# Optimization experiments

Hardware: AMD Instinct MI355X
Metric: run time of the kernel (lower is better)

## Reference

```python
import jax, jax.numpy as jnp
import numpy as np
import math

B, L, D, H, DFF, GEOM = 4, 768, 512, 8, 2048, 7
DK = D // H


def layer_norm(x, scale, bias, eps=1e-5):
    mu = jnp.mean(x, axis=-1, keepdims=True)
    var = jnp.mean(jnp.square(x - mu), axis=-1, keepdims=True)
    return (x - mu) * jax.lax.rsqrt(var + eps) * scale + bias


def setup_inputs() -> dict:
    key = jax.random.key(0)
    ks = jax.random.split(key, 20)
    s = 0.02
    inp = {
        "x": jax.random.normal(ks[0], (B, L, D), jnp.float32),
        "geom_feat": jax.random.uniform(ks[1], (B, L, L, GEOM), jnp.float32),
        "mask": jnp.ones((B, L), jnp.int32),
        # weights stored (in, out): y = x @ W + b, math-equivalent to torch Linear
        "Wq": jax.random.normal(ks[2], (D, D), jnp.float32) * s,
        "bq": jnp.zeros((D,), jnp.float32),
        "Wk": jax.random.normal(ks[3], (D, D), jnp.float32) * s,
        "bk": jnp.zeros((D,), jnp.float32),
        "Wv": jax.random.normal(ks[4], (D, D), jnp.float32) * s,
        "bv": jnp.zeros((D,), jnp.float32),
        "Wo": jax.random.normal(ks[5], (D, D), jnp.float32) * s,
        "bo": jnp.zeros((D,), jnp.float32),
        "Wg": jax.random.normal(ks[6], (GEOM, H), jnp.float32) * s,
        "bg": jnp.zeros((H,), jnp.float32),
        "Wgcn": jax.random.normal(ks[7], (D, D), jnp.float32) * s,
        "bgcn": jnp.zeros((D,), jnp.float32),
        "gcn_gate": jnp.float32(0.5),
        "W1": jax.random.normal(ks[8], (D, 2 * DFF), jnp.float32) * s,
        "b1": jnp.zeros((2 * DFF,), jnp.float32),
        "W2": jax.random.normal(ks[9], (DFF, D), jnp.float32) * s,
        "b2": jnp.zeros((D,), jnp.float32),
        "ln1_s": jnp.ones((D,), jnp.float32),
        "ln1_b": jnp.zeros((D,), jnp.float32),
        "ln2_s": jnp.ones((D,), jnp.float32),
        "ln2_b": jnp.zeros((D,), jnp.float32),
    }
    return inp


def reference(x, geom_feat, mask,
              Wq, bq, Wk, bk, Wv, bv, Wo, bo, Wg, bg,
              Wgcn, bgcn, gcn_gate, W1, b1, W2, b2,
              ln1_s, ln1_b, ln2_s, ln2_b):
    m = mask.astype(x.dtype)  # (B, L)
    # normalized adjacency from distance channel
    adj = jnp.exp(-geom_feat[..., 0] / 5.0)                 # (B, L, L)
    adj = adj * (m[:, :, None] * m[:, None, :])
    adj = adj / (jnp.sum(adj, axis=-1, keepdims=True) + 1e-6)

    h = layer_norm(x, ln1_s, ln1_b)                          # (B, L, D)

    # structure-guided attention
    Q = (h @ Wq + bq).reshape(B, L, H, DK)
    K = (h @ Wk + bk).reshape(B, L, H, DK)
    V = (h @ Wv + bv).reshape(B, L, H, DK)
    scores = jnp.einsum('blhd,bmhd->bhlm', Q, K) / math.sqrt(DK)
    bias = jnp.einsum('blmg,gh->bhlm', geom_feat, Wg) + bg[None, :, None, None]
    scores = scores + bias
    scores = jnp.where(mask[:, None, None, :] == 0, -10000.0, scores)
    attn = jax.nn.softmax(scores, axis=-1)
    ctx = jnp.einsum('bhlm,bmhd->blhd', attn, V).reshape(B, L, D)
    attn_out = ctx @ Wo + bo

    # dense GCN branch (exact GELU, matching torch nn.GELU default)
    g = h @ Wgcn + bgcn
    gcn_out = jax.nn.gelu(jnp.einsum('blm,bmd->bld', adj, g), approximate=False)

    x = x + attn_out + gcn_out * gcn_gate

    # gated feed-forward
    h2 = layer_norm(x, ln2_s, ln2_b)
    ff = h2 @ W1 + b1
    u, gate = ff[..., :DFF], ff[..., DFF:]
    x = x + (u * jax.nn.sigmoid(gate)) @ W2 + b2
    return x
```

## Files before the change

kernel.cpp:

```cpp
#include <hip/hip_runtime.h>
#include <hip/hip_bf16.h>
#include <math.h>

typedef __attribute__((ext_vector_type(8))) short bf8;
typedef __attribute__((ext_vector_type(4))) float f4;

__device__ __forceinline__ ushort f2bf(float x){
  union { float f; unsigned u; } v; v.f = x;
  unsigned r = (v.u + 0x7fffu + ((v.u >> 16) & 1u)) >> 16;
  return (ushort)r;
}
__device__ __forceinline__ float bf2f(ushort b){
  union { unsigned u; float f; } v; v.u = ((unsigned)b) << 16;
  return v.f;
}

struct GP {
  const ushort* A; long lda; long aBatch; long aHead;
  const ushort* Bt; long ldb; long bBatch; long bHead;
  const ushort* Bt2;
  int K; int zdiv;
  float* outf; ushort* outb;
  ushort* o1; ushort* o2; ushort* o3;
  const float* bias0; const float* bias1; const float* bias2; const float* bias3;
  const float* addf;
};

enum { EP_QKVG=0, EP_GCN, EP_ATTNOUT, EP_FF, EP_FINAL };

template<int EPI, bool DUAL>
__global__ __launch_bounds__(256)
void gemm_k(GP p) {
  __shared__ __align__(16) ushort As[64*64];
  __shared__ __align__(16) ushort Bs[64*64];
  __shared__ __align__(16) ushort Bs2[DUAL ? 64*64 : 8];
  const int tid = threadIdx.x;
  const int lane = tid & 63, wave = tid >> 6;
  const int wm = wave >> 1, wn = wave & 1;
  const int bm = blockIdx.x, bn = blockIdx.y, z = blockIdx.z;
  const int zb = z / p.zdiv, zh = z % p.zdiv;
  const ushort* Ab  = p.A  + (long)zb*p.aBatch + (long)zh*p.aHead + (long)bm*64*p.lda;
  const ushort* Btb = p.Bt + (long)zb*p.bBatch + (long)zh*p.bHead + (long)bn*64*p.ldb;
  const ushort* Bt2b = DUAL ? (p.Bt2 + (long)bn*64*p.ldb) : (const ushort*)nullptr;

  f4 acc[2][2] = {};
  f4 acc2[2][2] = {};

  const int sr = tid >> 3, sc = tid & 7;
  const int g = lane >> 4, lr = lane & 15;

  for (int k0 = 0; k0 < p.K; k0 += 64) {
    #pragma unroll
    for (int i = 0; i < 2; ++i) {
      int row = sr + i*32;
      int sw = (sc ^ (row & 7)) * 8;
      *(uint4*)&As[row*64 + sw] = *(const uint4*)(Ab  + (long)row*p.lda + k0 + sc*8);
      *(uint4*)&Bs[row*64 + sw] = *(const uint4*)(Btb + (long)row*p.ldb + k0 + sc*8);
      if (DUAL)
        *(uint4*)&Bs2[row*64 + sw] = *(const uint4*)(Bt2b + (long)row*p.ldb + k0 + sc*8);
    }
    __syncthreads();
    #pragma unroll
    for (int kw = 0; kw < 2; ++kw) {
      bf8 af[2], bfr[2], bf2[2];
      int chunk = kw*4 + g;
      #pragma unroll
      for (int f = 0; f < 2; ++f) {
        int ar = wm*32 + f*16 + lr;
        af[f]  = *(const bf8*)&As[ar*64 + ((chunk ^ (ar & 7)) * 8)];
        int br = wn*32 + f*16 + lr;
        bfr[f] = *(const bf8*)&Bs[br*64 + ((chunk ^ (br & 7)) * 8)];
        if (DUAL) bf2[f] = *(const bf8*)&Bs2[br*64 + ((chunk ^ (br & 7)) * 8)];
      }
      #pragma unroll
      for (int fm = 0; fm < 2; ++fm)
        #pragma unroll
        for (int fn = 0; fn < 2; ++fn) {
          acc[fm][fn] = __builtin_amdgcn_mfma_f32_16x16x32_bf16(af[fm], bfr[fn], acc[fm][fn], 0,0,0);
          if (DUAL) acc2[fm][fn] = __builtin_amdgcn_mfma_f32_16x16x32_bf16(af[fm], bf2[fn], acc2[fm][fn], 0,0,0);
        }
    }
    __syncthreads();
  }

  #pragma unroll
  for (int fm = 0; fm < 2; ++fm)
  #pragma unroll
  for (int fn = 0; fn < 2; ++fn)
  #pragma unroll
  for (int i = 0; i < 4; ++i) {
    int grow = bm*64 + wm*32 + fm*16 + g*4 + i;
    int gcol = bn*64 + wn*32 + fn*16 + lr;
    float v = acc[fm][fn][i];
    if constexpr (EPI == EP_QKVG) {
      int sec = gcol >> 9, cc = gcol & 511;
      const float* bp = sec==0 ? p.bias0 : sec==1 ? p.bias1 : sec==2 ? p.bias2 : p.bias3;
      v += bp[cc];
      ushort bvv = f2bf(v);
      if (sec == 0)      p.outb[(long)grow*512 + cc] = bvv;
      else if (sec == 1) p.o1[(long)grow*512 + cc] = bvv;
      else {
        int b = grow / 768, l = grow - b*768;
        ushort* dst = (sec==2) ? p.o2 : p.o3;
        dst[((long)b*512 + cc)*768 + l] = bvv;
      }
    } else if constexpr (EPI == EP_GCN) {
      float ge = 0.5f * v * (1.f + erff(v * 0.70710678118f));
      p.outf[((long)z*768 + grow)*512 + gcol] = ge;
    } else if constexpr (EPI == EP_ATTNOUT) {
      p.outf[(long)grow*512 + gcol] = v + p.bias0[gcol];
    } else if constexpr (EPI == EP_FF) {
      float u = v + p.bias0[gcol];
      float gt = acc2[fm][fn][i] + p.bias0[2048 + gcol];
      float a = u / (1.f + expf(-gt));
      p.outb[(long)grow*2048 + gcol] = f2bf(a);
    } else if constexpr (EPI == EP_FINAL) {
      long idx = (long)grow*512 + gcol;
      p.outf[idx] = p.addf[idx] + v + p.bias0[gcol];
    }
  }
}

__global__ __launch_bounds__(256) void flash_k(const ushort* __restrict__ qg,
    const ushort* __restrict__ kg, const ushort* __restrict__ vtg,
    const ushort* __restrict__ biasg, ushort* __restrict__ ctx) {
  __shared__ __align__(16) ushort Ks[64*64];
  __shared__ __align__(16) ushort Vs[64*64];
  __shared__ __align__(16) ushort Ps[64*64];
  const int tid = threadIdx.x;
  const int lane = tid & 63, w = tid >> 6;
  const int g = lane >> 4, lr = lane & 15;
  const int qt = blockIdx.x, bh = blockIdx.y;
  const int b = bh >> 3, h = bh & 7;
  const int q0 = qt*64;

  bf8 aq[2];
  #pragma unroll
  for (int kk = 0; kk < 2; ++kk)
    aq[kk] = *(const bf8*)&qg[(long)(b*768 + q0 + w*16 + lr)*512 + h*64 + kk*32 + g*8];

  f4 o[4] = {};
  float mrow[4], lsum[4];
  #pragma unroll
  for (int i = 0; i < 4; ++i) { mrow[i] = -1e30f; lsum[i] = 0.f; }

  const int srow = tid >> 3, sc = tid & 7;

  for (int kt = 0; kt < 12; ++kt) {
    const int kbase = kt*64;
    #pragma unroll
    for (int ps = 0; ps < 2; ++ps) {
      int r = srow + ps*32;
      int sw = ((sc ^ (r & 7)) * 8);
      *(uint4*)&Ks[r*64 + sw] = *(const uint4*)&kg[(long)(b*768 + kbase + r)*512 + h*64 + sc*8];
      *(uint4*)&Vs[r*64 + sw] = *(const uint4*)&vtg[((long)b*512 + h*64 + r)*768 + kbase + sc*8];
    }
    __syncthreads();

    f4 s[4] = {};
    #pragma unroll
    for (int kn = 0; kn < 4; ++kn) {
      #pragma unroll
      for (int kk = 0; kk < 2; ++kk) {
        int row = kn*16 + lr;
        bf8 bk = *(const bf8*)&Ks[row*64 + (((kk*4+g) ^ (row & 7)) * 8)];
        s[kn] = __builtin_amdgcn_mfma_f32_16x16x32_bf16(aq[kk], bk, s[kn], 0,0,0);
      }
    }

    float pv[4][4];
    #pragma unroll
    for (int kn = 0; kn < 4; ++kn)
      #pragma unroll
      for (int i = 0; i < 4; ++i) {
        float bv = bf2f(biasg[((long)bh*768 + q0 + w*16 + g*4 + i)*768 + kbase + kn*16 + lr]);
        pv[kn][i] = s[kn][i]*0.125f + bv;
      }

    #pragma unroll
    for (int i = 0; i < 4; ++i) {
      float m2 = fmaxf(fmaxf(pv[0][i], pv[1][i]), fmaxf(pv[2][i], pv[3][i]));
      #pragma unroll
      for (int off = 1; off < 16; off <<= 1) m2 = fmaxf(m2, __shfl_xor(m2, off, 64));
      float mnew = fmaxf(mrow[i], m2);
      float scale = __expf(mrow[i] - mnew);
      mrow[i] = mnew;
      float psum = 0.f;
      #pragma unroll
      for (int kn = 0; kn < 4; ++kn) { pv[kn][i] = __expf(pv[kn][i] - mnew); psum += pv[kn][i]; }
      #pragma unroll
      for (int off = 1; off < 16; off <<= 1) psum += __shfl_xor(psum, off, 64);
      lsum[i] = lsum[i]*scale + psum;
      #pragma unroll
      for (int dn = 0; dn < 4; ++dn) o[dn][i] *= scale;
    }

    #pragma unroll
    for (int kn = 0; kn < 4; ++kn)
      #pragma unroll
      for (int i = 0; i < 4; ++i) {
        int row = w*16 + g*4 + i;
        int col = kn*16 + lr;
        Ps[row*64 + (((col >> 3) ^ (row & 7)) * 8) + (col & 7)] = f2bf(pv[kn][i]);
      }

    #pragma unroll
    for (int kk2 = 0; kk2 < 2; ++kk2) {
      int prow = w*16 + lr;
      bf8 pa = *(const bf8*)&Ps[prow*64 + (((kk2*4+g) ^ (prow & 7)) * 8)];
      #pragma unroll
      for (int dn = 0; dn < 4; ++dn) {
        int vrow = dn*16 + lr;
        bf8 bv = *(const bf8*)&Vs[vrow*64 + (((kk2*4+g) ^ (vrow & 7)) * 8)];
        o[dn] = __builtin_amdgcn_mfma_f32_16x16x32_bf16(pa, bv, o[dn], 0,0,0);
      }
    }
    __syncthreads();
  }

  #pragma unroll
  for (int i = 0; i < 4; ++i) {
    float inv = 1.f / lsum[i];
    #pragma unroll
    for (int dn = 0; dn < 4; ++dn)
      ctx[(long)(b*768 + q0 + w*16 + g*4 + i)*512 + h*64 + dn*16 + lr] = f2bf(o[dn][i]*inv);
  }
}

__global__ __launch_bounds__(256) void transpose_bf(const float* src, ushort* dst, int R, int C) {
  __shared__ float t[32][33];
  int r0 = blockIdx.x*32, c0 = blockIdx.y*32;
  int tr = threadIdx.x >> 5, tc = threadIdx.x & 31;
  #pragma unroll
  for (int i = 0; i < 4; ++i)
    t[tr + i*8][tc] = src[(long)(r0 + tr + i*8)*C + c0 + tc];
  __syncthreads();
  #pragma unroll
  for (int i = 0; i < 4; ++i)
    dst[(long)(c0 + tr + i*8)*R + r0 + tc] = f2bf(t[tc][tr + i*8]);
}

__global__ __launch_bounds__(256) void ln_k(const float* x, const float* gam, const float* bet, ushort* out) {
  int row = blockIdx.x, tid = threadIdx.x;
  long base = (long)row*512;
  float v0 = x[base+tid], v1 = x[base+tid+256];
  float s = v0+v1, q = v0*v0 + v1*v1;
  #pragma unroll
  for (int off=32; off>=1; off>>=1){ s += __shfl_down(s,off,64); q += __shfl_down(q,off,64); }
  __shared__ float red[8];
  int lane=tid&63, wave=tid>>6;
  if (lane==0){ red[wave]=s; red[4+wave]=q; }
  __syncthreads();
  if (tid==0){ red[0]=red[0]+red[1]+red[2]+red[3]; red[4]=red[4]+red[5]+red[6]+red[7]; }
  __syncthreads();
  float mu = red[0]*(1.f/512.f);
  float var = red[4]*(1.f/512.f) - mu*mu;
  float rs = rsqrtf(var + 1e-5f);
  out[base+tid]     = f2bf((v0-mu)*rs*gam[tid]     + bet[tid]);
  out[base+tid+256] = f2bf((v1-mu)*rs*gam[tid+256] + bet[tid+256]);
}

__global__ __launch_bounds__(256) void resid_ln2_k(const float* x, const float* ao, const float* gc,
    const float* gatep, const float* gam, const float* bet, float* xmid, ushort* h2) {
  int row = blockIdx.x, tid = threadIdx.x;
  long base = (long)row*512;
  float gate = *gatep;
  float v0 = x[base+tid]     + ao[base+tid]     + gc[base+tid]*gate;
  float v1 = x[base+tid+256] + ao[base+tid+256] + gc[base+tid+256]*gate;
  xmid[base+tid] = v0; xmid[base+tid+256] = v1;
  float s = v0+v1, q = v0*v0 + v1*v1;
  #pragma unroll
  for (int off=32; off>=1; off>>=1){ s += __shfl_down(s,off,64); q += __shfl_down(q,off,64); }
  __shared__ float red[8];
  int lane=tid&63, wave=tid>>6;
  if (lane==0){ red[wave]=s; red[4+wave]=q; }
  __syncthreads();
  if (tid==0){ red[0]=red[0]+red[1]+red[2]+red[3]; red[4]=red[4]+red[5]+red[6]+red[7]; }
  __syncthreads();
  float mu = red[0]*(1.f/512.f);
  float var = red[4]*(1.f/512.f) - mu*mu;
  float rs = rsqrtf(var + 1e-5f);
  h2[base+tid]     = f2bf((v0-mu)*rs*gam[tid]     + bet[tid]);
  h2[base+tid+256] = f2bf((v1-mu)*rs*gam[tid+256] + bet[tid+256]);
}

__global__ __launch_bounds__(256) void adjbias_k(const float* __restrict__ geom,
    const int* __restrict__ mask, const float* __restrict__ Wg, const float* __restrict__ bg,
    ushort* __restrict__ adjb, ushort* __restrict__ biasb) {
  int bl = blockIdx.x;
  int b = bl / 768, l = bl - b*768;
  int tid = threadIdx.x;
  __shared__ float wgs[56];
  __shared__ float bgs[8];
  if (tid < 56) wgs[tid] = Wg[tid];
  if (tid < 8)  bgs[tid] = bg[tid];
  __syncthreads();
  float ml = (float)mask[bl];
  float e[3]; float ssum = 0.f;
  #pragma unroll
  for (int j = 0; j < 3; ++j) {
    int m = tid + j*256;
    const float* gp = &geom[((long)bl*768 + m)*7];
    float g0 = gp[0], g1 = gp[1], g2 = gp[2], g3 = gp[3], g4 = gp[4], g5 = gp[5], g6 = gp[6];
    float mm = (float)mask[b*768 + m];
    e[j] = __expf(-g0*0.2f) * mm;
    ssum += e[j];
    #pragma unroll
    for (int hh = 0; hh < 8; ++hh) {
      float bv = bgs[hh] + g0*wgs[hh] + g1*wgs[8+hh] + g2*wgs[16+hh] + g3*wgs[24+hh]
               + g4*wgs[32+hh] + g5*wgs[40+hh] + g6*wgs[48+hh];
      biasb[((long)(b*8+hh)*768 + l)*768 + m] = f2bf(mm != 0.f ? bv : -10000.f);
    }
  }
  #pragma unroll
  for (int off=32; off>=1; off>>=1) ssum += __shfl_down(ssum, off, 64);
  __shared__ float red[4];
  int lane = tid & 63, wave = tid >> 6;
  if (lane == 0) red[wave] = ssum;
  __syncthreads();
  if (tid == 0) red[0] = red[0]+red[1]+red[2]+red[3];
  __syncthreads();
  float inv = ml / (ml*red[0] + 1e-6f);
  #pragma unroll
  for (int j = 0; j < 3; ++j)
    adjb[(long)bl*768 + tid + j*256] = f2bf(e[j] * inv);
}

extern "C" void kernel_launch(void* const* d_in, const int* in_sizes, int n_in,
                              void* d_out, int out_size, void* d_ws, size_t ws_size,
                              hipStream_t stream) {
  const float* x    = (const float*)d_in[0];
  const float* geom = (const float*)d_in[1];
  const int*   mask = (const int*)d_in[2];
  const float* Wq   = (const float*)d_in[3];
  const float* bq   = (const float*)d_in[4];
  const float* Wk   = (const float*)d_in[5];
  const float* bk   = (const float*)d_in[6];
  const float* Wv   = (const float*)d_in[7];
  const float* bv   = (const float*)d_in[8];
  const float* Wo   = (const float*)d_in[9];
  const float* bo   = (const float*)d_in[10];
  const float* Wg   = (const float*)d_in[11];
  const float* bg   = (const float*)d_in[12];
  const float* Wgcn = (const float*)d_in[13];
  const float* bgcn = (const float*)d_in[14];
  const float* gate = (const float*)d_in[15];
  const float* W1   = (const float*)d_in[16];
  const float* b1   = (const float*)d_in[17];
  const float* W2   = (const float*)d_in[18];
  const float* b2   = (const float*)d_in[19];
  const float* ln1s = (const float*)d_in[20];
  const float* ln1b = (const float*)d_in[21];
  const float* ln2s = (const float*)d_in[22];
  const float* ln2b = (const float*)d_in[23];
  float* out = (float*)d_out;

  char* wp = (char*)d_ws;
  auto alloc = [&](size_t bytes)->char* { char* r = wp; wp += (bytes + 255) & ~(size_t)255; return r; };
  ushort* wqkvgT = (ushort*)alloc(2048*512*2);
  ushort* woT    = (ushort*)alloc(512*512*2);
  ushort* w1T    = (ushort*)alloc(4096*512*2);
  ushort* w2T    = (ushort*)alloc(512*2048*2);
  ushort* hbf    = (ushort*)alloc(3072*512*2);
  ushort* qbf    = (ushort*)alloc(3072*512*2);
  ushort* kbf    = (ushort*)alloc(3072*512*2);
  ushort* vt     = (ushort*)alloc((size_t)4*512*768*2);
  ushort* gt     = (ushort*)alloc((size_t)4*512*768*2);
  ushort* adjb   = (ushort*)alloc((size_t)4*768*768*2);
  ushort* biasb  = (ushort*)alloc((size_t)32*768*768*2);
  ushort* ctx    = (ushort*)alloc(3072*512*2);
  float*  aout   = (float*)alloc(3072*512*4);
  float*  gcnr   = (float*)alloc(3072*512*4);
  float*  xmid   = (float*)alloc(3072*512*4);
  ushort* h2bf   = (ushort*)alloc(3072*512*2);
  ushort* act    = biasb;

  transpose_bf<<<dim3(16,16), 256, 0, stream>>>(Wq,   wqkvgT + 0*512*512, 512, 512);
  transpose_bf<<<dim3(16,16), 256, 0, stream>>>(Wk,   wqkvgT + 1*512*512, 512, 512);
  transpose_bf<<<dim3(16,16), 256, 0, stream>>>(Wv,   wqkvgT + 2*512*512, 512, 512);
  transpose_bf<<<dim3(16,16), 256, 0, stream>>>(Wgcn, wqkvgT + 3*512*512, 512, 512);
  transpose_bf<<<dim3(16,16), 256, 0, stream>>>(Wo,   woT, 512, 512);
  transpose_bf<<<dim3(16,128),256, 0, stream>>>(W1,   w1T, 512, 4096);
  transpose_bf<<<dim3(64,16), 256, 0, stream>>>(W2,   w2T, 2048, 512);

  ln_k<<<3072, 256, 0, stream>>>(x, ln1s, ln1b, hbf);

  adjbias_k<<<3072, 256, 0, stream>>>(geom, mask, Wg, bg, adjb, biasb);

  GP p{};
  p.A = hbf; p.lda = 512; p.aBatch = 0; p.aHead = 0;
  p.Bt = wqkvgT; p.ldb = 512; p.bBatch = 0; p.bHead = 0;
  p.K = 512; p.zdiv = 1;
  p.outb = qbf; p.o1 = kbf; p.o2 = vt; p.o3 = gt;
  p.bias0 = bq; p.bias1 = bk; p.bias2 = bv; p.bias3 = bgcn;
  gemm_k<EP_QKVG,false><<<dim3(48,32,1), 256, 0, stream>>>(p);

  flash_k<<<dim3(12,32), 256, 0, stream>>>(qbf, kbf, vt, biasb, ctx);

  p = GP{};
  p.A = adjb; p.lda = 768; p.aBatch = (long)768*768; p.aHead = 0;
  p.Bt = gt; p.ldb = 768; p.bBatch = (long)512*768; p.bHead = 0;
  p.K = 768; p.zdiv = 1;
  p.outf = gcnr;
  gemm_k<EP_GCN,false><<<dim3(12,8,4), 256, 0, stream>>>(p);

  p = GP{};
  p.A = ctx; p.lda = 512; p.aBatch = 0; p.aHead = 0;
  p.Bt = woT; p.ldb = 512; p.bBatch = 0; p.bHead = 0;
  p.K = 512; p.zdiv = 1;
  p.outf = aout; p.bias0 = bo;
  gemm_k<EP_ATTNOUT,false><<<dim3(48,8,1), 256, 0, stream>>>(p);

  resid_ln2_k<<<3072, 256, 0, stream>>>(x, aout, gcnr, gate, ln2s, ln2b, xmid, h2bf);

  p = GP{};
  p.A = h2bf; p.lda = 512; p.aBatch = 0; p.aHead = 0;
  p.Bt = w1T; p.ldb = 512; p.bBatch = 0; p.bHead = 0;
  p.Bt2 = w1T + (long)2048*512;
  p.K = 512; p.zdiv = 1;
  p.outb = act; p.bias0 = b1;
  gemm_k<EP_FF,true><<<dim3(48,32,1), 256, 0, stream>>>(p);

  p = GP{};
  p.A = act; p.lda = 2048; p.aBatch = 0; p.aHead = 0;
  p.Bt = w2T; p.ldb = 2048; p.bBatch = 0; p.bHead = 0;
  p.K = 2048; p.zdiv = 1;
  p.outf = out; p.bias0 = b2; p.addf = xmid;
  gemm_k<EP_FINAL,false><<<dim3(48,8,1), 256, 0, stream>>>(p);
}
```

Before: 313.7 us.

## Enlarge GEMM tiles to 128-row blocks and load tiles via direct global-to-LDS

```diff
diff --git a/kernel.cpp b/kernel.cpp
--- a/kernel.cpp
+++ b/kernel.cpp
@@ -4,6 +4,9 @@
 
 typedef __attribute__((ext_vector_type(8))) short bf8;
 typedef __attribute__((ext_vector_type(4))) float f4;
+
+typedef const __attribute__((address_space(1))) void* gas_t;
+typedef __attribute__((address_space(3))) void* las_t;
 
 __device__ __forceinline__ ushort f2bf(float x){
   union { float f; unsigned u; } v; v.f = x;
@@ -16,10 +19,10 @@
 }
 
 struct GP {
-  const ushort* A; long lda; long aBatch; long aHead;
-  const ushort* Bt; long ldb; long bBatch; long bHead;
+  const ushort* A; long lda; long aBatch;
+  const ushort* Bt; long ldb; long bBatch;
   const ushort* Bt2;
-  int K; int zdiv;
+  int K;
   float* outf; ushort* outb;
   ushort* o1; ushort* o2; ushort* o3;
   const float* bias0; const float* bias1; const float* bias2; const float* bias3;
@@ -28,54 +31,74 @@
 
 enum { EP_QKVG=0, EP_GCN, EP_ATTNOUT, EP_FF, EP_FINAL };
 
-template<int EPI, bool DUAL>
+template<int EPI, bool DUAL, int BN>
 __global__ __launch_bounds__(256)
 void gemm_k(GP p) {
-  __shared__ __align__(16) ushort As[64*64];
-  __shared__ __align__(16) ushort Bs[64*64];
-  __shared__ __align__(16) ushort Bs2[DUAL ? 64*64 : 8];
+  constexpr int WMW = (BN==128) ? 2 : 4;
+  constexpr int WNW = (BN==128) ? 2 : 1;
+  constexpr int WM = 128/WMW, WN = BN/WNW;
+  constexpr int MF = WM/16, NF = WN/16;
+  constexpr int BI = BN/32;
+  __shared__ __align__(16) ushort As[128*64];
+  __shared__ __align__(16) ushort Bs[BN*64];
+  __shared__ __align__(16) ushort Bs2[DUAL ? BN*64 : 8];
   const int tid = threadIdx.x;
-  const int lane = tid & 63, wave = tid >> 6;
-  const int wm = wave >> 1, wn = wave & 1;
+  const int lane = tid & 63, w = tid >> 6;
+  const int wm = (WNW==1) ? w : (w >> 1);
+  const int wn = (WNW==1) ? 0 : (w & 1);
+  const int g = lane >> 4, lr = lane & 15;
+  const int lr8 = lane >> 3, sc = lane & 7;
   const int bm = blockIdx.x, bn = blockIdx.y, z = blockIdx.z;
-  const int zb = z / p.zdiv, zh = z % p.zdiv;
-  const ushort* Ab  = p.A  + (long)zb*p.aBatch + (long)zh*p.aHead + (long)bm*64*p.lda;
-  const ushort* Btb = p.Bt + (long)zb*p.bBatch + (long)zh*p.bHead + (long)bn*64*p.ldb;
-  const ushort* Bt2b = DUAL ? (p.Bt2 + (long)bn*64*p.ldb) : (const ushort*)nullptr;
-
-  f4 acc[2][2] = {};
-  f4 acc2[2][2] = {};
-
-  const int sr = tid >> 3, sc = tid & 7;
-  const int g = lane >> 4, lr = lane & 15;
+
+  const ushort* Ab  = p.A  + (long)z*p.aBatch + (long)bm*128*p.lda;
+  const ushort* Btb = p.Bt + (long)z*p.bBatch + (long)bn*BN*p.ldb;
+  const ushort* Bt2b = DUAL ? (p.Bt2 + (long)bn*BN*p.ldb) : (const ushort*)nullptr;
+
+  f4 acc[MF][NF] = {};
+  f4 acc2[DUAL?MF:1][DUAL?NF:1] = {};
 
   for (int k0 = 0; k0 < p.K; k0 += 64) {
     #pragma unroll
-    for (int i = 0; i < 2; ++i) {
-      int row = sr + i*32;
-      int sw = (sc ^ (row & 7)) * 8;
-      *(uint4*)&As[row*64 + sw] = *(const uint4*)(Ab  + (long)row*p.lda + k0 + sc*8);
-      *(uint4*)&Bs[row*64 + sw] = *(const uint4*)(Btb + (long)row*p.ldb + k0 + sc*8);
-      if (DUAL)
-        *(uint4*)&Bs2[row*64 + sw] = *(const uint4*)(Bt2b + (long)row*p.ldb + k0 + sc*8);
+    for (int i = 0; i < 4; ++i) {
+      int row = i*32 + w*8 + lr8;
+      const ushort* gs = Ab + (long)row*p.lda + k0 + ((sc ^ (row & 7)) << 3);
+      __builtin_amdgcn_global_load_lds((gas_t)gs, (las_t)&As[i*2048 + w*512], 16, 0, 0);
+    }
+    #pragma unroll
+    for (int i = 0; i < BI; ++i) {
+      int row = i*32 + w*8 + lr8;
+      const ushort* gs = Btb + (long)row*p.ldb + k0 + ((sc ^ (row & 7)) << 3);
+      __builtin_amdgcn_global_load_lds((gas_t)gs, (las_t)&Bs[i*2048 + w*512], 16, 0, 0);
+    }
+    if (DUAL) {
+      #pragma unroll
+      for (int i = 0; i < BI; ++i) {
+        int row = i*32 + w*8 + lr8;
+        const ushort* gs = Bt2b + (long)row*p.ldb + k0 + ((sc ^ (row & 7)) << 3);
+        __builtin_amdgcn_global_load_lds((gas_t)gs, (las_t)&Bs2[i*2048 + w*512], 16, 0, 0);
+      }
     }
     __syncthreads();
+
     #pragma unroll
     for (int kw = 0; kw < 2; ++kw) {
-      bf8 af[2], bfr[2], bf2[2];
-      int chunk = kw*4 + g;
-      #pragma unroll
-      for (int f = 0; f < 2; ++f) {
-        int ar = wm*32 + f*16 + lr;
-        af[f]  = *(const bf8*)&As[ar*64 + ((chunk ^ (ar & 7)) * 8)];
-        int br = wn*32 + f*16 + lr;
-        bfr[f] = *(const bf8*)&Bs[br*64 + ((chunk ^ (br & 7)) * 8)];
-        if (DUAL) bf2[f] = *(const bf8*)&Bs2[br*64 + ((chunk ^ (br & 7)) * 8)];
-      }
-      #pragma unroll
-      for (int fm = 0; fm < 2; ++fm)
+      const int chunk = kw*4 + g;
+      bf8 af[MF], bfr[NF], bf2[DUAL?NF:1];
+      #pragma unroll
+      for (int f = 0; f < MF; ++f) {
+        int ar = wm*WM + f*16 + lr;
+        af[f] = *(const bf8*)&As[ar*64 + ((chunk ^ (ar & 7)) << 3)];
+      }
+      #pragma unroll
+      for (int f = 0; f < NF; ++f) {
+        int br = wn*WN + f*16 + lr;
+        bfr[f] = *(const bf8*)&Bs[br*64 + ((chunk ^ (br & 7)) << 3)];
+        if (DUAL) bf2[f] = *(const bf8*)&Bs2[br*64 + ((chunk ^ (br & 7)) << 3)];
+      }
+      #pragma unroll
+      for (int fm = 0; fm < MF; ++fm)
         #pragma unroll
-        for (int fn = 0; fn < 2; ++fn) {
+        for (int fn = 0; fn < NF; ++fn) {
           acc[fm][fn] = __builtin_amdgcn_mfma_f32_16x16x32_bf16(af[fm], bfr[fn], acc[fm][fn], 0,0,0);
           if (DUAL) acc2[fm][fn] = __builtin_amdgcn_mfma_f32_16x16x32_bf16(af[fm], bf2[fn], acc2[fm][fn], 0,0,0);
         }
@@ -84,13 +107,13 @@
   }
 
   #pragma unroll
-  for (int fm = 0; fm < 2; ++fm)
-  #pragma unroll
-  for (int fn = 0; fn < 2; ++fn)
+  for (int fm = 0; fm < MF; ++fm)
+  #pragma unroll
+  for (int fn = 0; fn < NF; ++fn)
   #pragma unroll
   for (int i = 0; i < 4; ++i) {
-    int grow = bm*64 + wm*32 + fm*16 + g*4 + i;
-    int gcol = bn*64 + wn*32 + fn*16 + lr;
+    int grow = bm*128 + wm*WM + fm*16 + g*4 + i;
+    int gcol = bn*BN + wn*WN + fn*16 + lr;
     float v = acc[fm][fn][i];
     if constexpr (EPI == EP_QKVG) {
       int sec = gcol >> 9, cc = gcol & 511;
@@ -384,47 +407,46 @@
   transpose_bf<<<dim3(64,16), 256, 0, stream>>>(W2,   w2T, 2048, 512);
 
   ln_k<<<3072, 256, 0, stream>>>(x, ln1s, ln1b, hbf);
-
   adjbias_k<<<3072, 256, 0, stream>>>(geom, mask, Wg, bg, adjb, biasb);
 
   GP p{};
-  p.A = hbf; p.lda = 512; p.aBatch = 0; p.aHead = 0;
-  p.Bt = wqkvgT; p.ldb = 512; p.bBatch = 0; p.bHead = 0;
-  p.K = 512; p.zdiv = 1;
+  p.A = hbf; p.lda = 512; p.aBatch = 0;
+  p.Bt = wqkvgT; p.ldb = 512; p.bBatch = 0;
+  p.K = 512;
   p.outb = qbf; p.o1 = kbf; p.o2 = vt; p.o3 = gt;
   p.bias0 = bq; p.bias1 = bk; p.bias2 = bv; p.bias3 = bgcn;
-  gemm_k<EP_QKVG,false><<<dim3(48,32,1), 256, 0, stream>>>(p);
+  gemm_k<EP_QKVG,false,128><<<dim3(24,16,1), 256, 0, stream>>>(p);
 
   flash_k<<<dim3(12,32), 256, 0, stream>>>(qbf, kbf, vt, biasb, ctx);
 
   p = GP{};
-  p.A = adjb; p.lda = 768; p.aBatch = (long)768*768; p.aHead = 0;
-  p.Bt = gt; p.ldb = 768; p.bBatch = (long)512*768; p.bHead = 0;
-  p.K = 768; p.zdiv = 1;
+  p.A = adjb; p.lda = 768; p.aBatch = (long)768*768;
+  p.Bt = gt; p.ldb = 768; p.bBatch = (long)512*768;
+  p.K = 768;
   p.outf = gcnr;
-  gemm_k<EP_GCN,false><<<dim3(12,8,4), 256, 0, stream>>>(p);
+  gemm_k<EP_GCN,false,128><<<dim3(6,4,4), 256, 0, stream>>>(p);
 
   p = GP{};
-  p.A = ctx; p.lda = 512; p.aBatch = 0; p.aHead = 0;
-  p.Bt = woT; p.ldb = 512; p.bBatch = 0; p.bHead = 0;
-  p.K = 512; p.zdiv = 1;
+  p.A = ctx; p.lda = 512; p.aBatch = 0;
+  p.Bt = woT; p.ldb = 512; p.bBatch = 0;
+  p.K = 512;
   p.outf = aout; p.bias0 = bo;
-  gemm_k<EP_ATTNOUT,false><<<dim3(48,8,1), 256, 0, stream>>>(p);
+  gemm_k<EP_ATTNOUT,false,128><<<dim3(24,4,1), 256, 0, stream>>>(p);
 
   resid_ln2_k<<<3072, 256, 0, stream>>>(x, aout, gcnr, gate, ln2s, ln2b, xmid, h2bf);
 
   p = GP{};
-  p.A = h2bf; p.lda = 512; p.aBatch = 0; p.aHead = 0;
-  p.Bt = w1T; p.ldb = 512; p.bBatch = 0; p.bHead = 0;
+  p.A = h2bf; p.lda = 512; p.aBatch = 0;
+  p.Bt = w1T; p.ldb = 512; p.bBatch = 0;
   p.Bt2 = w1T + (long)2048*512;
-  p.K = 512; p.zdiv = 1;
+  p.K = 512;
   p.outb = act; p.bias0 = b1;
-  gemm_k<EP_FF,true><<<dim3(48,32,1), 256, 0, stream>>>(p);
+  gemm_k<EP_FF,true,64><<<dim3(24,32,1), 256, 0, stream>>>(p);
 
   p = GP{};
-  p.A = act; p.lda = 2048; p.aBatch = 0; p.aHead = 0;
-  p.Bt = w2T; p.ldb = 2048; p.bBatch = 0; p.bHead = 0;
-  p.K = 2048; p.zdiv = 1;
+  p.A = act; p.lda = 2048; p.aBatch = 0;
+  p.Bt = w2T; p.ldb = 2048; p.bBatch = 0;
+  p.K = 2048;
   p.outf = out; p.bias0 = b2; p.addf = xmid;
-  gemm_k<EP_FINAL,false><<<dim3(48,8,1), 256, 0, stream>>>(p);
-}
+  gemm_k<EP_FINAL,false,128><<<dim3(24,4,1), 256, 0, stream>>>(p);
+}
```

After: 392.0 us. +25.0%, slower.
